# Kernel optimization log

Hardware: AMD Instinct MI355X
Metric: run time of the kernel (lower is better)

The kernel has to match this reference:

```python
import jax, jax.numpy as jnp
import numpy as np

K, M, N = 8, 1024, 1024  # bits, in_features, out_features (nf)
B_, S_ = 4, 2048

def setup_inputs() -> dict:
    key = jax.random.key(0)
    k1, k2, k3, k4 = jax.random.split(key, 4)
    x = jax.random.normal(k1, (B_, S_, M), dtype=jnp.float32)
    # per-bit +/-1 sign matrices, stored as float (module casts int8 -> x.dtype)
    binary = jnp.where(jax.random.normal(k2, (K, M, N)) > 0, 1.0, -1.0).astype(jnp.float32)
    # positive per-bit, per-output-channel scales (sup decomposition yields positives)
    scale = jax.random.uniform(k3, (K, 1, N), dtype=jnp.float32, minval=0.01, maxval=1.0)
    bias = jax.random.normal(k4, (N,), dtype=jnp.float32)
    return {"x": x, "binary": binary, "scale": scale, "bias": bias}

def reference(x, binary, scale, bias):
    size_out = x.shape[:-1] + (N,)
    x2 = x.reshape(-1, x.shape[-1])                 # [T, m]
    # k separate dense matmuls against +/-1 matrices: [k, T, n]
    xk = jnp.einsum('tm,kmn->ktn', x2, binary)
    out = jnp.sum(xk * scale, axis=0)               # per-bit scale then sum over bits
    out = out + bias
    return out.reshape(size_out)
```

## Files before the change

### kernel.cpp

```cpp
#include <hip/hip_runtime.h>
#include <cstdint>

#define TDIM 8192
#define MDIM 1024
#define NDIM 1024
#define KBITS 8
#define BK 64
#define BT 256
#define BN 128
#define NTILES (MDIM / BK)

typedef __bf16 bf16x8 __attribute__((ext_vector_type(8)));
typedef float f32x4 __attribute__((ext_vector_type(4)));

#define GAS(p) ((__attribute__((address_space(1))) void*)(uintptr_t)(p))
#define LAS(p) ((__attribute__((address_space(3))) void*)(uintptr_t)(p))

__device__ __forceinline__ unsigned short f2bf(float f) {
    union { float f; unsigned u; } v; v.f = f;
    unsigned r = v.u + 0x7fffu + ((v.u >> 16) & 1u);
    return (unsigned short)(r >> 16);
}

__global__ __launch_bounds__(256) void prep_kernel(const float* __restrict__ x,
                                                   unsigned short* __restrict__ xb,
                                                   const float* __restrict__ binary,
                                                   const float* __restrict__ scale,
                                                   unsigned short* __restrict__ wtr) {
    __shared__ float tile[32][33];
    const int tid = threadIdx.x;
    if (blockIdx.x >= 1024) {
        size_t idx = ((size_t)(blockIdx.x - 1024) * 256 + tid) * 8;
        float4 a = *(const float4*)(x + idx);
        float4 b = *(const float4*)(x + idx + 4);
        uint4 o;
        o.x = (unsigned)f2bf(a.x) | ((unsigned)f2bf(a.y) << 16);
        o.y = (unsigned)f2bf(a.z) | ((unsigned)f2bf(a.w) << 16);
        o.z = (unsigned)f2bf(b.x) | ((unsigned)f2bf(b.y) << 16);
        o.w = (unsigned)f2bf(b.z) | ((unsigned)f2bf(b.w) << 16);
        *(uint4*)(xb + idx) = o;
        return;
    }
    const int n0 = (blockIdx.x & 31) * 32;
    const int m0 = (blockIdx.x >> 5) * 32;
    const int r = tid >> 3;
    const int cn = (tid & 7) * 4;
    f32x4 acc = {0.f, 0.f, 0.f, 0.f};
#pragma unroll
    for (int k = 0; k < KBITS; ++k) {
        f32x4 v = *(const f32x4*)(binary + ((size_t)k * MDIM + m0 + r) * NDIM + n0 + cn);
        f32x4 s = *(const f32x4*)(scale + (size_t)k * NDIM + n0 + cn);
        acc += v * s;
    }
#pragma unroll
    for (int e = 0; e < 4; ++e) tile[cn + e][r] = acc[e];
    __syncthreads();
    const int rn = tid >> 3;
    const int cm = (tid & 7) * 4;
    ushort4 o4;
    o4.x = f2bf(tile[rn][cm + 0]);
    o4.y = f2bf(tile[rn][cm + 1]);
    o4.z = f2bf(tile[rn][cm + 2]);
    o4.w = f2bf(tile[rn][cm + 3]);
    *(ushort4*)(wtr + (size_t)(n0 + rn) * MDIM + m0 + cm) = o4;
}

__global__ __launch_bounds__(512, 2) void gemm_kernel(const unsigned short* __restrict__ xb,
                                                      const unsigned short* __restrict__ wtr,
                                                      const float* __restrict__ bias,
                                                      float* __restrict__ out) {
    constexpr int ASZ = BT * BK;
    constexpr int BSZ = BN * BK;
    constexpr int BUF = ASZ + BSZ;
    __shared__ __attribute__((aligned(16))) unsigned short lds[3 * BUF];

    const int tid = threadIdx.x;
    const int lane = tid & 63;
    const int wv = tid >> 6;
    const int wm = wv >> 1;
    const int wn = wv & 1;
    const int lrow = lane & 15;
    const int q = lane >> 4;

    const int t0 = blockIdx.x * BT;
    const int n0 = blockIdx.y * BN;

    const unsigned short* srcA[4];
    int dstA[4];
    const unsigned short* srcB[2];
    int dstB[2];
#pragma unroll
    for (int j = 0; j < 4; ++j) {
        int s = tid + j * 512;
        int r = s >> 3;
        int g = (s & 7) ^ (r & 7);
        srcA[j] = xb + (size_t)(t0 + r) * MDIM + g * 8;
        dstA[j] = s * 8;
    }
#pragma unroll
    for (int j = 0; j < 2; ++j) {
        int s = tid + j * 512;
        int r = s >> 3;
        int g = (s & 7) ^ (r & 7);
        srcB[j] = wtr + (size_t)(n0 + r) * MDIM + g * 8;
        dstB[j] = ASZ + s * 8;
    }

    int a_off[2][4], b_off[2][4];
#pragma unroll
    for (int h = 0; h < 2; ++h)
#pragma unroll
        for (int i = 0; i < 4; ++i) {
            int m = wm * 64 + i * 16 + lrow;
            a_off[h][i] = (m * 8 + ((h * 4 + q) ^ (m & 7))) * 8;
            int n = wn * 64 + i * 16 + lrow;
            b_off[h][i] = ASZ + (n * 8 + ((h * 4 + q) ^ (n & 7))) * 8;
        }

    f32x4 acc[4][4];
    const f32x4 zero = {0.f, 0.f, 0.f, 0.f};
#pragma unroll
    for (int i = 0; i < 4; ++i)
#pragma unroll
        for (int j = 0; j < 4; ++j) acc[i][j] = zero;

    auto stage = [&](int bufsel, int t) {
        unsigned short* bb = lds + bufsel * BUF;
        const int k0 = t * BK;
#pragma unroll
        for (int j = 0; j < 4; ++j)
            __builtin_amdgcn_global_load_lds(GAS(srcA[j] + k0), LAS(bb + dstA[j]), 16, 0, 0);
#pragma unroll
        for (int j = 0; j < 2; ++j)
            __builtin_amdgcn_global_load_lds(GAS(srcB[j] + k0), LAS(bb + dstB[j]), 16, 0, 0);
    };

    stage(0, 0);
    stage(1, 1);
    asm volatile("s_waitcnt vmcnt(6)" ::: "memory");
    __builtin_amdgcn_s_barrier();
    __builtin_amdgcn_sched_barrier(0);

#pragma unroll
    for (int t = 0; t < NTILES; ++t) {
        const int cur = t % 3;
        if (t + 2 < NTILES) stage((t + 2) % 3, t + 2);

        const unsigned short* base = lds + cur * BUF;
#pragma unroll
        for (int h = 0; h < 2; ++h) {
            bf16x8 af[4], bfr[4];
#pragma unroll
            for (int i = 0; i < 4; ++i) af[i] = *(const bf16x8*)(base + a_off[h][i]);
#pragma unroll
            for (int i = 0; i < 4; ++i) bfr[i] = *(const bf16x8*)(base + b_off[h][i]);
            __builtin_amdgcn_s_setprio(1);
#pragma unroll
            for (int i = 0; i < 4; ++i)
#pragma unroll
                for (int j = 0; j < 4; ++j)
                    acc[i][j] = __builtin_amdgcn_mfma_f32_16x16x32_bf16(af[i], bfr[j],
                                                                        acc[i][j], 0, 0, 0);
            __builtin_amdgcn_s_setprio(0);
        }

        if (t + 1 < NTILES) {
            if (t + 2 < NTILES) {
                asm volatile("s_waitcnt vmcnt(6)" ::: "memory");
            } else {
                asm volatile("s_waitcnt vmcnt(0)" ::: "memory");
            }
            __builtin_amdgcn_s_barrier();
            __builtin_amdgcn_sched_barrier(0);
        }
    }

#pragma unroll
    for (int j = 0; j < 4; ++j) {
        const int n = n0 + wn * 64 + j * 16 + lrow;
        const float bv = bias[n];
#pragma unroll
        for (int i = 0; i < 4; ++i) {
            const int tb = t0 + wm * 64 + i * 16 + q * 4;
#pragma unroll
            for (int r = 0; r < 4; ++r) {
                out[(size_t)(tb + r) * NDIM + n] = acc[i][j][r] + bv;
            }
        }
    }
}

extern "C" void kernel_launch(void* const* d_in, const int* in_sizes, int n_in,
                              void* d_out, int out_size, void* d_ws, size_t ws_size,
                              hipStream_t stream) {
    const float* x      = (const float*)d_in[0];
    const float* binary = (const float*)d_in[1];
    const float* scale  = (const float*)d_in[2];
    const float* bias   = (const float*)d_in[3];
    float* out = (float*)d_out;

    unsigned short* xb  = (unsigned short*)d_ws;
    unsigned short* wtr = xb + (size_t)TDIM * MDIM;

    prep_kernel<<<1024 + 4096, 256, 0, stream>>>(x, xb, binary, scale, wtr);
    gemm_kernel<<<dim3(TDIM / BT, NDIM / BN), 512, 0, stream>>>(xb, wtr, bias, out);
}
```

Measured before the change: 123.5 us.

## Fuse fp32-to-bf16 conversion of x into GEMM A-tile loading

Drops the separate pass that converted x to bf16 in workspace. The GEMM now loads fp32 x into registers, converts it and writes bf16 into LDS itself, and the pipeline goes from a three-stage direct-to-LDS ring to double buffering with register staging. This saves a full write and re-read of the bf16 copy of x. In exchange x is re-read as fp32 by every N-block (8x, at twice the bytes), there is a full vmcnt(0) wait every tile, and the prefetch depth is shallower.

```diff
diff --git a/kernel.cpp b/kernel.cpp
--- a/kernel.cpp
+++ b/kernel.cpp
@@ -22,25 +22,11 @@
     return (unsigned short)(r >> 16);
 }
 
-__global__ __launch_bounds__(256) void prep_kernel(const float* __restrict__ x,
-                                                   unsigned short* __restrict__ xb,
-                                                   const float* __restrict__ binary,
-                                                   const float* __restrict__ scale,
-                                                   unsigned short* __restrict__ wtr) {
+__global__ __launch_bounds__(256) void wfold_kernel(const float* __restrict__ binary,
+                                                    const float* __restrict__ scale,
+                                                    unsigned short* __restrict__ wtr) {
     __shared__ float tile[32][33];
     const int tid = threadIdx.x;
-    if (blockIdx.x >= 1024) {
-        size_t idx = ((size_t)(blockIdx.x - 1024) * 256 + tid) * 8;
-        float4 a = *(const float4*)(x + idx);
-        float4 b = *(const float4*)(x + idx + 4);
-        uint4 o;
-        o.x = (unsigned)f2bf(a.x) | ((unsigned)f2bf(a.y) << 16);
-        o.y = (unsigned)f2bf(a.z) | ((unsigned)f2bf(a.w) << 16);
-        o.z = (unsigned)f2bf(b.x) | ((unsigned)f2bf(b.y) << 16);
-        o.w = (unsigned)f2bf(b.z) | ((unsigned)f2bf(b.w) << 16);
-        *(uint4*)(xb + idx) = o;
-        return;
-    }
     const int n0 = (blockIdx.x & 31) * 32;
     const int m0 = (blockIdx.x >> 5) * 32;
     const int r = tid >> 3;
@@ -65,14 +51,14 @@
     *(ushort4*)(wtr + (size_t)(n0 + rn) * MDIM + m0 + cm) = o4;
 }
 
-__global__ __launch_bounds__(512, 2) void gemm_kernel(const unsigned short* __restrict__ xb,
+__global__ __launch_bounds__(512, 2) void gemm_kernel(const float* __restrict__ x,
                                                       const unsigned short* __restrict__ wtr,
                                                       const float* __restrict__ bias,
                                                       float* __restrict__ out) {
     constexpr int ASZ = BT * BK;
     constexpr int BSZ = BN * BK;
     constexpr int BUF = ASZ + BSZ;
-    __shared__ __attribute__((aligned(16))) unsigned short lds[3 * BUF];
+    __shared__ __attribute__((aligned(16))) unsigned short lds[2 * BUF];
 
     const int tid = threadIdx.x;
     const int lane = tid & 63;
@@ -85,7 +71,7 @@
     const int t0 = blockIdx.x * BT;
     const int n0 = blockIdx.y * BN;
 
-    const unsigned short* srcA[4];
+    const float* srcA[4];
     int dstA[4];
     const unsigned short* srcB[2];
     int dstB[2];
@@ -94,7 +80,7 @@
         int s = tid + j * 512;
         int r = s >> 3;
         int g = (s & 7) ^ (r & 7);
-        srcA[j] = xb + (size_t)(t0 + r) * MDIM + g * 8;
+        srcA[j] = x + (size_t)(t0 + r) * MDIM + g * 8;
         dstA[j] = s * 8;
     }
 #pragma unroll
@@ -124,27 +110,49 @@
 #pragma unroll
         for (int j = 0; j < 4; ++j) acc[i][j] = zero;
 
-    auto stage = [&](int bufsel, int t) {
+    f32x4 ar[4][2];
+
+    auto issueA = [&](int t) {
+        const int k0 = t * BK;
+#pragma unroll
+        for (int j = 0; j < 4; ++j) {
+            ar[j][0] = *(const f32x4*)(srcA[j] + k0);
+            ar[j][1] = *(const f32x4*)(srcA[j] + k0 + 4);
+        }
+    };
+    auto issueB = [&](int bufsel, int t) {
         unsigned short* bb = lds + bufsel * BUF;
         const int k0 = t * BK;
-#pragma unroll
-        for (int j = 0; j < 4; ++j)
-            __builtin_amdgcn_global_load_lds(GAS(srcA[j] + k0), LAS(bb + dstA[j]), 16, 0, 0);
 #pragma unroll
         for (int j = 0; j < 2; ++j)
             __builtin_amdgcn_global_load_lds(GAS(srcB[j] + k0), LAS(bb + dstB[j]), 16, 0, 0);
     };
-
-    stage(0, 0);
-    stage(1, 1);
-    asm volatile("s_waitcnt vmcnt(6)" ::: "memory");
-    __builtin_amdgcn_s_barrier();
-    __builtin_amdgcn_sched_barrier(0);
+    auto writeA = [&](int bufsel) {
+        unsigned short* bb = lds + bufsel * BUF;
+#pragma unroll
+        for (int j = 0; j < 4; ++j) {
+            uint4 o;
+            o.x = (unsigned)f2bf(ar[j][0][0]) | ((unsigned)f2bf(ar[j][0][1]) << 16);
+            o.y = (unsigned)f2bf(ar[j][0][2]) | ((unsigned)f2bf(ar[j][0][3]) << 16);
+            o.z = (unsigned)f2bf(ar[j][1][0]) | ((unsigned)f2bf(ar[j][1][1]) << 16);
+            o.w = (unsigned)f2bf(ar[j][1][2]) | ((unsigned)f2bf(ar[j][1][3]) << 16);
+            *(uint4*)(bb + dstA[j]) = o;
+        }
+    };
+
+    issueA(0);
+    issueB(0, 0);
+    asm volatile("s_waitcnt vmcnt(0)" ::: "memory");
+    writeA(0);
+    __syncthreads();
 
 #pragma unroll
     for (int t = 0; t < NTILES; ++t) {
-        const int cur = t % 3;
-        if (t + 2 < NTILES) stage((t + 2) % 3, t + 2);
+        const int cur = t & 1;
+        if (t + 1 < NTILES) {
+            issueA(t + 1);
+            issueB(cur ^ 1, t + 1);
+        }
 
         const unsigned short* base = lds + cur * BUF;
 #pragma unroll
@@ -165,13 +173,9 @@
         }
 
         if (t + 1 < NTILES) {
-            if (t + 2 < NTILES) {
-                asm volatile("s_waitcnt vmcnt(6)" ::: "memory");
-            } else {
-                asm volatile("s_waitcnt vmcnt(0)" ::: "memory");
-            }
-            __builtin_amdgcn_s_barrier();
-            __builtin_amdgcn_sched_barrier(0);
+            asm volatile("s_waitcnt vmcnt(0)" ::: "memory");
+            writeA(cur ^ 1);
+            __syncthreads();
         }
     }
 
@@ -199,9 +203,8 @@
     const float* bias   = (const float*)d_in[3];
     float* out = (float*)d_out;
 
-    unsigned short* xb  = (unsigned short*)d_ws;
-    unsigned short* wtr = xb + (size_t)TDIM * MDIM;
-
-    prep_kernel<<<1024 + 4096, 256, 0, stream>>>(x, xb, binary, scale, wtr);
-    gemm_kernel<<<dim3(TDIM / BT, NDIM / BN), 512, 0, stream>>>(xb, wtr, bias, out);
-}
+    unsigned short* wtr = (unsigned short*)d_ws;
+
+    wfold_kernel<<<1024, 256, 0, stream>>>(binary, scale, wtr);
+    gemm_kernel<<<dim3(TDIM / BT, NDIM / BN), 512, 0, stream>>>(x, wtr, bias, out);
+}
```

After: 133.1 us. +7.8%, slower.

## Interleave global-to-LDS prefetch with MFMA phases using ping-pong barriers

Applied to the files above, without the earlier changes.

Splits each K-tile into two phases. Each phase loads its LDS fragments, issues part of the next-next tile's global_load_lds prefetch, then synchronizes with barriers around the MFMA block. The intent is to spread memory issue across the compute and align the waves so loads and MFMAs from different waves overlap. It adds extra s_barrier and lgkmcnt waits per half-tile, which can add stalls.

```diff
diff --git a/kernel.cpp b/kernel.cpp
--- a/kernel.cpp
+++ b/kernel.cpp
@@ -124,7 +124,7 @@
 #pragma unroll
         for (int j = 0; j < 4; ++j) acc[i][j] = zero;
 
-    auto stage = [&](int bufsel, int t) {
+    auto stage_all = [&](int bufsel, int t) {
         unsigned short* bb = lds + bufsel * BUF;
         const int k0 = t * BK;
 #pragma unroll
@@ -135,25 +135,63 @@
             __builtin_amdgcn_global_load_lds(GAS(srcB[j] + k0), LAS(bb + dstB[j]), 16, 0, 0);
     };
 
-    stage(0, 0);
-    stage(1, 1);
+    stage_all(0, 0);
+    stage_all(1, 1);
     asm volatile("s_waitcnt vmcnt(6)" ::: "memory");
     __builtin_amdgcn_s_barrier();
     __builtin_amdgcn_sched_barrier(0);
 
 #pragma unroll
     for (int t = 0; t < NTILES; ++t) {
-        const int cur = t % 3;
-        if (t + 2 < NTILES) stage((t + 2) % 3, t + 2);
-
-        const unsigned short* base = lds + cur * BUF;
-#pragma unroll
-        for (int h = 0; h < 2; ++h) {
+        const unsigned short* base = lds + (t % 3) * BUF;
+        unsigned short* sbuf = lds + ((t + 2) % 3) * BUF;
+        const int k2 = (t + 2) * BK;
+        const bool prefetch = (t + 2 < NTILES);
+
+        {
             bf16x8 af[4], bfr[4];
 #pragma unroll
-            for (int i = 0; i < 4; ++i) af[i] = *(const bf16x8*)(base + a_off[h][i]);
-#pragma unroll
-            for (int i = 0; i < 4; ++i) bfr[i] = *(const bf16x8*)(base + b_off[h][i]);
+            for (int i = 0; i < 4; ++i) af[i] = *(const bf16x8*)(base + a_off[0][i]);
+#pragma unroll
+            for (int i = 0; i < 4; ++i) bfr[i] = *(const bf16x8*)(base + b_off[0][i]);
+            if (prefetch) {
+#pragma unroll
+                for (int j = 0; j < 3; ++j)
+                    __builtin_amdgcn_global_load_lds(GAS(srcA[j] + k2),
+                                                     LAS(sbuf + dstA[j]), 16, 0, 0);
+            }
+            __builtin_amdgcn_s_barrier();
+            asm volatile("s_waitcnt lgkmcnt(0)" ::: "memory");
+            __builtin_amdgcn_sched_barrier(0);
+            __builtin_amdgcn_s_setprio(1);
+#pragma unroll
+            for (int i = 0; i < 4; ++i)
+#pragma unroll
+                for (int j = 0; j < 4; ++j)
+                    acc[i][j] = __builtin_amdgcn_mfma_f32_16x16x32_bf16(af[i], bfr[j],
+                                                                        acc[i][j], 0, 0, 0);
+            __builtin_amdgcn_s_setprio(0);
+            __builtin_amdgcn_s_barrier();
+            __builtin_amdgcn_sched_barrier(0);
+        }
+
+        {
+            bf16x8 af[4], bfr[4];
+#pragma unroll
+            for (int i = 0; i < 4; ++i) af[i] = *(const bf16x8*)(base + a_off[1][i]);
+#pragma unroll
+            for (int i = 0; i < 4; ++i) bfr[i] = *(const bf16x8*)(base + b_off[1][i]);
+            if (prefetch) {
+                __builtin_amdgcn_global_load_lds(GAS(srcA[3] + k2),
+                                                 LAS(sbuf + dstA[3]), 16, 0, 0);
+#pragma unroll
+                for (int j = 0; j < 2; ++j)
+                    __builtin_amdgcn_global_load_lds(GAS(srcB[j] + k2),
+                                                     LAS(sbuf + dstB[j]), 16, 0, 0);
+            }
+            __builtin_amdgcn_s_barrier();
+            asm volatile("s_waitcnt lgkmcnt(0)" ::: "memory");
+            __builtin_amdgcn_sched_barrier(0);
             __builtin_amdgcn_s_setprio(1);
 #pragma unroll
             for (int i = 0; i < 4; ++i)
```

Result: no change. 123.9 us (+0.3%).
